# Kernel tuning notes

Hardware: AMD Instinct MI355X
Metric: run time of the kernel (lower is better)

The kernel has to match this reference:

```python
import jax, jax.numpy as jnp
import numpy as np

HEADS = 8
DIM_HEAD = 32
DIM = 256           # must equal HEADS*DIM_HEAD (required by the torch view)
HIDDEN = HEADS * DIM_HEAD
NUM_GROUPS = 32
EPS = 1e-6


def setup_inputs() -> dict:
    key = jax.random.key(0)
    ks = jax.random.split(key, 6)
    b, c, h, w = 16, DIM, 64, 64
    x = jax.random.normal(ks[0], (b, c, h, w), dtype=jnp.float32)
    # conv1x1 weights stored as 2D matrices (out_ch, in_ch)
    w_qkv = jax.random.normal(ks[1], (3 * HIDDEN, DIM), dtype=jnp.float32) * (1.0 / np.sqrt(DIM))
    w_out = jax.random.normal(ks[2], (DIM, HIDDEN), dtype=jnp.float32) * (1.0 / np.sqrt(HIDDEN))
    b_out = jax.random.normal(ks[3], (DIM,), dtype=jnp.float32) * 0.01
    gn_gamma = jnp.ones((DIM,), dtype=jnp.float32)
    gn_beta = jnp.zeros((DIM,), dtype=jnp.float32)
    return {"x": x, "w_qkv": w_qkv, "w_out": w_out, "b_out": b_out,
            "gn_gamma": gn_gamma, "gn_beta": gn_beta}


def _group_norm(x, gamma, beta):
    # GroupNorm32: compute in float32, eps=1e-6, affine
    b, c, h, w = x.shape
    g = NUM_GROUPS
    xf = x.astype(jnp.float32).reshape(b, g, c // g, h, w)
    mean = xf.mean(axis=(2, 3, 4), keepdims=True)
    var = xf.var(axis=(2, 3, 4), keepdims=True)
    xn = (xf - mean) * jax.lax.rsqrt(var + EPS)
    xn = xn.reshape(b, c, h, w)
    return (xn * gamma[None, :, None, None] + beta[None, :, None, None]).astype(x.dtype)


def reference(x, w_qkv, w_out, b_out, gn_gamma, gn_beta):
    b, c, h, w = x.shape
    n = h * w
    # qkv projection (1x1 conv == matmul over channels)
    qkv = jnp.einsum('oc,bchw->bohw', w_qkv, x)            # (b, 3*hidden, h, w)
    qkv = qkv.reshape(b, 3, HEADS, DIM_HEAD, n)
    q, k, v = qkv[:, 0], qkv[:, 1], qkv[:, 2]              # (b, h, d, n)
    q = jax.nn.softmax(q, axis=-2)                         # softmax over feature dim
    k = jax.nn.softmax(k, axis=-1)                         # softmax over spatial dim
    context = jnp.einsum('bhdn,bhen->bhde', k, v)          # (b, heads, d, d)
    out = jnp.einsum('bhde,bhdn->bhen', context, q)        # (b, heads, d, n)
    out = out.reshape(b, c, h, w)
    out = jnp.einsum('oc,bchw->bohw', w_out, out) + b_out[None, :, None, None]
    out = _group_norm(out, gn_gamma, gn_beta)
    return out + x
```

## Files before the change

### kernel.cpp

```cpp
#include <hip/hip_runtime.h>


typedef short s8v __attribute__((ext_vector_type(8)));
typedef float f32x4 __attribute__((ext_vector_type(4)));

__device__ __forceinline__ short f2bf(float f) {
  union { float f; unsigned u; } v; v.f = f;
  unsigned r = v.u + 0x7FFF + ((v.u >> 16) & 1);
  return (short)(r >> 16);
}
__device__ __forceinline__ float bf2f(short h) {
  union { unsigned u; float f; } v; v.u = ((unsigned)(unsigned short)h) << 16;
  return v.f;
}
__device__ __forceinline__ void gld16(const short* g, short* l) {
  __builtin_amdgcn_global_load_lds(
      (const __attribute__((address_space(1))) unsigned*)g,
      (__attribute__((address_space(3))) unsigned*)l, 16, 0, 0);
}

__global__ __launch_bounds__(256) void cast_to_bf16(
    const float* __restrict__ src, short* __restrict__ dst, int n8) {
  int id = blockIdx.x * 256 + threadIdx.x;
  if (id >= n8) return;
  long off = (long)id * 8;
  float4 a = *(const float4*)&src[off];
  float4 b = *(const float4*)&src[off + 4];
  s8v o;
  o[0] = f2bf(a.x); o[1] = f2bf(a.y); o[2] = f2bf(a.z); o[3] = f2bf(a.w);
  o[4] = f2bf(b.x); o[5] = f2bf(b.y); o[6] = f2bf(b.z); o[7] = f2bf(b.w);
  *(s8v*)&dst[off] = o;
}

__global__ __launch_bounds__(256) void cast_transpose_x(
    const float* __restrict__ x, short* __restrict__ xt) {
  int b = blockIdx.z;
  int n0 = blockIdx.x * 64, c0 = blockIdx.y * 64;
  __shared__ short ls[64][65];
  int t = threadIdx.x;
  const float* xb = x + ((long)b * 256 + c0) * 4096 + n0;
  int ci = t >> 4, j4 = (t & 15) * 4;
#pragma unroll
  for (int i = 0; i < 4; ++i) {
    int cl = ci + i * 16;
    float4 v = *(const float4*)&xb[(long)cl * 4096 + j4];
    ls[j4 + 0][cl] = f2bf(v.x);
    ls[j4 + 1][cl] = f2bf(v.y);
    ls[j4 + 2][cl] = f2bf(v.z);
    ls[j4 + 3][cl] = f2bf(v.w);
  }
  __syncthreads();
  short* xtb = xt + ((long)b * 4096 + n0) * 256 + c0;
#pragma unroll
  for (int i = 0; i < 2; ++i) {
    int id = t + i * 256;
    int nl = id >> 3, c8 = (id & 7) * 8;
    s8v o;
#pragma unroll
    for (int e = 0; e < 8; ++e) o[e] = ls[nl][c8 + e];
    *(s8v*)&xtb[(long)nl * 256 + c8] = o;
  }
}

__global__ __launch_bounds__(256) void gemm_bf16(
    const short* __restrict__ A, const short* __restrict__ Bt,
    short* __restrict__ C, const float* __restrict__ bias,
    long a_bstride, int M) {
  __shared__ short lA[128 * 64];
  __shared__ short lB[128 * 64];
  int b = blockIdx.z;
  int mt = blockIdx.y * 128, nt = blockIdx.x * 128;
  int tid = threadIdx.x;
  int lane = tid & 63;
  int wm = tid >> 7, wn = (tid >> 6) & 1;
  const short* Ab = A + (long)b * a_bstride + (long)mt * 256;
  const short* Bb = Bt + ((long)b * 4096 + nt) * 256;
  short* Cb = C + ((long)b * M + mt) * 4096 + nt;

  f32x4 acc[4][4];
#pragma unroll
  for (int i = 0; i < 4; ++i)
#pragma unroll
    for (int j = 0; j < 4; ++j) acc[i][j] = (f32x4){0.f, 0.f, 0.f, 0.f};

  for (int k0 = 0; k0 < 256; k0 += 64) {
#pragma unroll
    for (int is = 0; is < 4; ++is) {
      int s = is * 256 + tid;
      int row = s >> 3, kcp = s & 7;
      int kcl = kcp ^ (row & 7);
      short* la = &lA[(is * 256 + (tid & ~63)) * 8];
      short* lb = &lB[(is * 256 + (tid & ~63)) * 8];
      gld16(Ab + (long)row * 256 + k0 + kcl * 8, la);
      gld16(Bb + (long)row * 256 + k0 + kcl * 8, lb);
    }
    asm volatile("s_waitcnt vmcnt(0)" ::: "memory");
    __syncthreads();
#pragma unroll
    for (int kw = 0; kw < 2; ++kw) {
      int kc = kw * 4 + (lane >> 4);
      int rl = lane & 15;
      s8v av[4], bv[4];
#pragma unroll
      for (int mi = 0; mi < 4; ++mi) {
        int row = wm * 64 + mi * 16 + rl;
        av[mi] = *(const s8v*)&lA[row * 64 + ((kc ^ (row & 7)) << 3)];
      }
#pragma unroll
      for (int ni = 0; ni < 4; ++ni) {
        int row = wn * 64 + ni * 16 + rl;
        bv[ni] = *(const s8v*)&lB[row * 64 + ((kc ^ (row & 7)) << 3)];
      }
#pragma unroll
      for (int mi = 0; mi < 4; ++mi)
#pragma unroll
        for (int ni = 0; ni < 4; ++ni)
          acc[mi][ni] = __builtin_amdgcn_mfma_f32_16x16x32_bf16(
              av[mi], bv[ni], acc[mi][ni], 0, 0, 0);
    }
    __syncthreads();
  }
#pragma unroll
  for (int mi = 0; mi < 4; ++mi) {
#pragma unroll
    for (int r = 0; r < 4; ++r) {
      int o = wm * 64 + mi * 16 + (lane >> 4) * 4 + r;
      float bvv = bias ? bias[mt + o] : 0.f;
#pragma unroll
      for (int ni = 0; ni < 4; ++ni) {
        int n = wn * 64 + ni * 16 + (lane & 15);
        Cb[(long)o * 4096 + n] = f2bf(acc[mi][ni][r] + bvv);
      }
    }
  }
}

__global__ __launch_bounds__(256) void softmax_qT(
    const short* __restrict__ qkv, short* __restrict__ qt) {
  int n = blockIdx.x * 256 + threadIdx.x;
  int h = blockIdx.y, b = blockIdx.z;
  const short* qb = qkv + ((long)b * 768 + h * 32) * 4096 + n;
  float v[32];
  float m = -1e30f;
#pragma unroll
  for (int d = 0; d < 32; ++d) { v[d] = bf2f(qb[(long)d * 4096]); m = fmaxf(m, v[d]); }
  float s = 0.f;
#pragma unroll
  for (int d = 0; d < 32; ++d) { v[d] = __expf(v[d] - m); s += v[d]; }
  float inv = 1.f / s;
  short* dst = qt + ((long)b * 4096 + n) * 256 + h * 32;
#pragma unroll
  for (int c8 = 0; c8 < 4; ++c8) {
    s8v o;
#pragma unroll
    for (int e = 0; e < 8; ++e) o[e] = f2bf(v[c8 * 8 + e] * inv);
    *(s8v*)&dst[c8 * 8] = o;
  }
}

__global__ __launch_bounds__(256) void ctx_mfma(
    const short* __restrict__ qkv, float* __restrict__ ctxp, float* __restrict__ sp) {
  int split = blockIdx.x;
  int h = blockIdx.y, b = blockIdx.z;
  int tid = threadIdx.x;
  int w = tid >> 6, l = tid & 63;
  const short* kb = qkv + ((long)(b * 768 + 256) + h * 32) * 4096;
  const short* vb = kb + (long)256 * 4096;
  int rl = l & 15, kg = l >> 4;
  int n_base = split * 1024 + w * 256;

  f32x4 acc[2][2];
#pragma unroll
  for (int i = 0; i < 2; ++i)
#pragma unroll
    for (int j = 0; j < 2; ++j) acc[i][j] = (f32x4){0.f, 0.f, 0.f, 0.f};
  float s_part0 = 0.f, s_part1 = 0.f;

#pragma unroll 2
  for (int it = 0; it < 8; ++it) {
    int n0 = n_base + it * 32 + kg * 8;
    s8v a0, a1, b0, b1;
    {
      s8v kr = *(const s8v*)&kb[(long)rl * 4096 + n0];
#pragma unroll
      for (int j = 0; j < 8; ++j) {
        float f = __expf(bf2f(kr[j]));
        s_part0 += f;
        a0[j] = f2bf(f);
      }
    }
    {
      s8v kr = *(const s8v*)&kb[(long)(16 + rl) * 4096 + n0];
#pragma unroll
      for (int j = 0; j < 8; ++j) {
        float f = __expf(bf2f(kr[j]));
        s_part1 += f;
        a1[j] = f2bf(f);
      }
    }
    b0 = *(const s8v*)&vb[(long)rl * 4096 + n0];
    b1 = *(const s8v*)&vb[(long)(16 + rl) * 4096 + n0];
    acc[0][0] = __builtin_amdgcn_mfma_f32_16x16x32_bf16(a0, b0, acc[0][0], 0, 0, 0);
    acc[0][1] = __builtin_amdgcn_mfma_f32_16x16x32_bf16(a0, b1, acc[0][1], 0, 0, 0);
    acc[1][0] = __builtin_amdgcn_mfma_f32_16x16x32_bf16(a1, b0, acc[1][0], 0, 0, 0);
    acc[1][1] = __builtin_amdgcn_mfma_f32_16x16x32_bf16(a1, b1, acc[1][1], 0, 0, 0);
  }
  s_part0 += __shfl_xor(s_part0, 16); s_part0 += __shfl_xor(s_part0, 32);
  s_part1 += __shfl_xor(s_part1, 16); s_part1 += __shfl_xor(s_part1, 32);

  __shared__ float lctx[4][1024];
  __shared__ float lsum[4][32];
#pragma unroll
  for (int di = 0; di < 2; ++di)
#pragma unroll
    for (int ei = 0; ei < 2; ++ei)
#pragma unroll
      for (int r = 0; r < 4; ++r) {
        int row = di * 16 + kg * 4 + r;
        int col = ei * 16 + rl;
        lctx[w][row * 32 + col] = acc[di][ei][r];
      }
  if (kg == 0) { lsum[w][rl] = s_part0; lsum[w][16 + rl] = s_part1; }
  __syncthreads();
  long base = (long)(b * 8 + h) * 4 + split;
#pragma unroll
  for (int i = 0; i < 4; ++i) {
    int id = tid + i * 256;
    ctxp[base * 1024 + id] = lctx[0][id] + lctx[1][id] + lctx[2][id] + lctx[3][id];
  }
  if (tid < 32)
    sp[base * 32 + tid] = lsum[0][tid] + lsum[1][tid] + lsum[2][tid] + lsum[3][tid];
}

__global__ __launch_bounds__(256) void make_wf(
    const float* __restrict__ ctxp, const float* __restrict__ sp,
    const float* __restrict__ w_out, short* __restrict__ wf) {
  int h = blockIdx.x, b = blockIdx.y;
  __shared__ float c[32][33];
  __shared__ float inv_s[32];
  __shared__ float wv[256][33];
  int t = threadIdx.x;
  long base = (long)(b * 8 + h) * 4;
#pragma unroll
  for (int i = 0; i < 4; ++i) {
    int id = t + i * 256;
    float v = ctxp[base * 1024 + id] + ctxp[(base + 1) * 1024 + id] +
              ctxp[(base + 2) * 1024 + id] + ctxp[(base + 3) * 1024 + id];
    c[id >> 5][id & 31] = v;
  }
  if (t < 32) {
    float sv = sp[base * 32 + t] + sp[(base + 1) * 32 + t] +
               sp[(base + 2) * 32 + t] + sp[(base + 3) * 32 + t];
    inv_s[t] = 1.f / sv;
  }
#pragma unroll
  for (int r = 0; r < 32; ++r) {
    int row = r * 8 + (t >> 5);
    wv[row][t & 31] = w_out[row * 256 + h * 32 + (t & 31)];
  }
  __syncthreads();
  float wr[32];
#pragma unroll
  for (int e = 0; e < 32; ++e) wr[e] = wv[t][e];
  float tmp[32];
#pragma unroll
  for (int dd = 0; dd < 32; ++dd) {
    float sum = 0.f;
#pragma unroll
    for (int e = 0; e < 32; ++e) sum += wr[e] * c[dd][e];
    tmp[dd] = sum * inv_s[dd];
  }
  short* dst = wf + ((long)b * 256 + t) * 256 + h * 32;
#pragma unroll
  for (int c8 = 0; c8 < 4; ++c8) {
    s8v o;
#pragma unroll
    for (int e = 0; e < 8; ++e) o[e] = f2bf(tmp[c8 * 8 + e]);
    *(s8v*)&dst[c8 * 8] = o;
  }
}

__global__ __launch_bounds__(256) void gn_stats(
    const short* __restrict__ lin, float2* __restrict__ stats) {
  int g = blockIdx.x, b = blockIdx.y;
  const short* base = lin + ((long)b * 256 + g * 8) * 4096;
  int t = threadIdx.x;
  float s = 0.f, ss = 0.f;
#pragma unroll
  for (int l = 0; l < 16; ++l) {
    s8v v = ((const s8v*)base)[t + l * 256];
#pragma unroll
    for (int e = 0; e < 8; ++e) { float f = bf2f(v[e]); s += f; ss += f * f; }
  }
  int wave = t >> 6, lane = t & 63;
#pragma unroll
  for (int off = 32; off >= 1; off >>= 1) { s += __shfl_xor(s, off); ss += __shfl_xor(ss, off); }
  __shared__ float rs[4], rss[4];
  if (lane == 0) { rs[wave] = s; rss[wave] = ss; }
  __syncthreads();
  if (t == 0) {
    s = rs[0] + rs[1] + rs[2] + rs[3];
    ss = rss[0] + rss[1] + rss[2] + rss[3];
    float mean = s * (1.f / 32768.f);
    float var = ss * (1.f / 32768.f) - mean * mean;
    stats[b * 32 + g] = make_float2(mean, rsqrtf(var + 1e-6f));
  }
}

__global__ __launch_bounds__(256) void final_out(
    const short* __restrict__ lin, const float* __restrict__ x,
    const float2* __restrict__ stats, const float* __restrict__ gamma,
    const float* __restrict__ beta, float* __restrict__ out) {
  long id = (long)blockIdx.x * 256 + threadIdx.x;
  long e0 = id * 8;
  int b = (int)(e0 >> 20);
  int rem = (int)(e0 & 1048575);
  int c = rem >> 12;
  float2 st = stats[b * 32 + (c >> 3)];
  float ga = gamma[c] * st.y;
  float be = beta[c] - st.x * ga;
  s8v l8 = *(const s8v*)&lin[e0];
  float4 x0 = *(const float4*)&x[e0];
  float4 x1 = *(const float4*)&x[e0 + 4];
  float4 o0, o1;
  o0.x = bf2f(l8[0]) * ga + be + x0.x;
  o0.y = bf2f(l8[1]) * ga + be + x0.y;
  o0.z = bf2f(l8[2]) * ga + be + x0.z;
  o0.w = bf2f(l8[3]) * ga + be + x0.w;
  o1.x = bf2f(l8[4]) * ga + be + x1.x;
  o1.y = bf2f(l8[5]) * ga + be + x1.y;
  o1.z = bf2f(l8[6]) * ga + be + x1.z;
  o1.w = bf2f(l8[7]) * ga + be + x1.w;
  *(float4*)&out[e0] = o0;
  *(float4*)&out[e0 + 4] = o1;
}

extern "C" void kernel_launch(void* const* d_in, const int* in_sizes, int n_in,
                              void* d_out, int out_size, void* d_ws, size_t ws_size,
                              hipStream_t stream) {
  const float* x     = (const float*)d_in[0];
  const float* w_qkv = (const float*)d_in[1];
  const float* w_out = (const float*)d_in[2];
  const float* b_out = (const float*)d_in[3];
  const float* gamma = (const float*)d_in[4];
  const float* beta  = (const float*)d_in[5];
  float* out = (float*)d_out;

  short* xt   = (short*)d_ws;
  short* qkvb = xt + 16777216;
  short* lin  = qkvb + 50331648;
  short* wqb  = lin + 16777216;
  short* wfb  = wqb + 196608;
  float* ctxp = (float*)(wfb + 1048576);
  float* sp   = ctxp + 524288;
  float2* stats = (float2*)(sp + 16384);

  cast_to_bf16<<<96, 256, 0, stream>>>(w_qkv, wqb, 24576);
  cast_transpose_x<<<dim3(64, 4, 16), 256, 0, stream>>>(x, xt);
  gemm_bf16<<<dim3(32, 6, 16), 256, 0, stream>>>(wqb, xt, qkvb, nullptr, 0, 768);
  softmax_qT<<<dim3(16, 8, 16), 256, 0, stream>>>(qkvb, xt);
  ctx_mfma<<<dim3(4, 8, 16), 256, 0, stream>>>(qkvb, ctxp, sp);
  make_wf<<<dim3(8, 16), 256, 0, stream>>>(ctxp, sp, w_out, wfb);
  gemm_bf16<<<dim3(32, 2, 16), 256, 0, stream>>>(wfb, xt, lin, b_out, 65536, 256);
  gn_stats<<<dim3(32, 16), 256, 0, stream>>>(lin, stats);
  final_out<<<8192, 256, 0, stream>>>(lin, x, stats, gamma, beta, out);
}
```

Measured before the change: 157.9 us.

## Fuse q-softmax into QKV GEMM epilogue and GroupNorm stats into output GEMM

The QKV GEMM now applies the feature-dim softmax to q tiles in its epilogue, using lane shuffles, and writes transposed q directly. This removes the separate softmax_qT pass and the write and re-read of q. The output GEMM accumulates GroupNorm sum and sum-of-squares with atomics in its epilogue, which replaces the gn_stats kernel; final_out now derives mean and rstd from those sums. Both GEMMs also double-buffer their LDS staging so global loads overlap the MFMA work. The costs are more LDS per block, nondeterministic atomic accumulation order, and an extra zeroing kernel.

Result: slower. 161.9 us (+2.5%).

```diff
diff --git a/kernel.cpp b/kernel.cpp
--- a/kernel.cpp
+++ b/kernel.cpp
@@ -32,6 +32,10 @@
   *(s8v*)&dst[off] = o;
 }
 
+__global__ __launch_bounds__(256) void zero_stats(float* __restrict__ p) {
+  p[blockIdx.x * 256 + threadIdx.x] = 0.f;
+}
+
 __global__ __launch_bounds__(256) void cast_transpose_x(
     const float* __restrict__ x, short* __restrict__ xt) {
   int b = blockIdx.z;
@@ -62,20 +66,19 @@
   }
 }
 
-__global__ __launch_bounds__(256) void gemm_bf16(
+__global__ __launch_bounds__(256) void gemm_qkv(
     const short* __restrict__ A, const short* __restrict__ Bt,
-    short* __restrict__ C, const float* __restrict__ bias,
-    long a_bstride, int M) {
-  __shared__ short lA[128 * 64];
-  __shared__ short lB[128 * 64];
+    short* __restrict__ kv, short* __restrict__ qT) {
+  __shared__ short lA[2][8192];
+  __shared__ short lB[2][8192];
   int b = blockIdx.z;
   int mt = blockIdx.y * 128, nt = blockIdx.x * 128;
   int tid = threadIdx.x;
   int lane = tid & 63;
   int wm = tid >> 7, wn = (tid >> 6) & 1;
-  const short* Ab = A + (long)b * a_bstride + (long)mt * 256;
+  int rl = lane & 15, kg = lane >> 4;
+  const short* Ab = A + (long)mt * 256;
   const short* Bb = Bt + ((long)b * 4096 + nt) * 256;
-  short* Cb = C + ((long)b * M + mt) * 4096 + nt;
 
   f32x4 acc[4][4];
 #pragma unroll
@@ -83,33 +86,41 @@
 #pragma unroll
     for (int j = 0; j < 4; ++j) acc[i][j] = (f32x4){0.f, 0.f, 0.f, 0.f};
 
-  for (int k0 = 0; k0 < 256; k0 += 64) {
+  auto stage = [&](int buf, int k0) {
 #pragma unroll
     for (int is = 0; is < 4; ++is) {
       int s = is * 256 + tid;
       int row = s >> 3, kcp = s & 7;
       int kcl = kcp ^ (row & 7);
-      short* la = &lA[(is * 256 + (tid & ~63)) * 8];
-      short* lb = &lB[(is * 256 + (tid & ~63)) * 8];
-      gld16(Ab + (long)row * 256 + k0 + kcl * 8, la);
-      gld16(Bb + (long)row * 256 + k0 + kcl * 8, lb);
-    }
-    asm volatile("s_waitcnt vmcnt(0)" ::: "memory");
-    __syncthreads();
+      gld16(Ab + (long)row * 256 + k0 + kcl * 8, &lA[buf][(is * 256 + (tid & ~63)) * 8]);
+      gld16(Bb + (long)row * 256 + k0 + kcl * 8, &lB[buf][(is * 256 + (tid & ~63)) * 8]);
+    }
+  };
+
+  stage(0, 0);
+#pragma unroll
+  for (int s = 0; s < 4; ++s) {
+    int cur = s & 1;
+    if (s < 3) {
+      stage(cur ^ 1, (s + 1) * 64);
+      asm volatile("s_waitcnt vmcnt(8)" ::: "memory");
+    } else {
+      asm volatile("s_waitcnt vmcnt(0)" ::: "memory");
+    }
+    __builtin_amdgcn_s_barrier();
 #pragma unroll
     for (int kw = 0; kw < 2; ++kw) {
-      int kc = kw * 4 + (lane >> 4);
-      int rl = lane & 15;
+      int kc = kw * 4 + kg;
       s8v av[4], bv[4];
 #pragma unroll
       for (int mi = 0; mi < 4; ++mi) {
         int row = wm * 64 + mi * 16 + rl;
-        av[mi] = *(const s8v*)&lA[row * 64 + ((kc ^ (row & 7)) << 3)];
+        av[mi] = *(const s8v*)&lA[cur][row * 64 + ((kc ^ (row & 7)) << 3)];
       }
 #pragma unroll
       for (int ni = 0; ni < 4; ++ni) {
         int row = wn * 64 + ni * 16 + rl;
-        bv[ni] = *(const s8v*)&lB[row * 64 + ((kc ^ (row & 7)) << 3)];
+        bv[ni] = *(const s8v*)&lB[cur][row * 64 + ((kc ^ (row & 7)) << 3)];
       }
 #pragma unroll
       for (int mi = 0; mi < 4; ++mi)
@@ -118,53 +129,170 @@
           acc[mi][ni] = __builtin_amdgcn_mfma_f32_16x16x32_bf16(
               av[mi], bv[ni], acc[mi][ni], 0, 0, 0);
     }
-    __syncthreads();
-  }
+    asm volatile("s_waitcnt lgkmcnt(0)" ::: "memory");
+    __builtin_amdgcn_s_barrier();
+  }
+
+  if (mt < 256) {
+    short* qTb = qT + ((long)b * 4096 + nt) * 256 + mt;
+#pragma unroll
+    for (int ni = 0; ni < 4; ++ni) {
+      int n = wn * 64 + ni * 16 + rl;
+#pragma unroll
+      for (int p = 0; p < 2; ++p) {
+        float v[8];
+        float m = -1e30f;
+#pragma unroll
+        for (int j = 0; j < 8; ++j) {
+          v[j] = acc[p * 2 + (j >> 2)][ni][j & 3];
+          m = fmaxf(m, v[j]);
+        }
+        m = fmaxf(m, __shfl_xor(m, 16));
+        m = fmaxf(m, __shfl_xor(m, 32));
+        float ssum = 0.f;
+#pragma unroll
+        for (int j = 0; j < 8; ++j) { v[j] = __expf(v[j] - m); ssum += v[j]; }
+        ssum += __shfl_xor(ssum, 16);
+        ssum += __shfl_xor(ssum, 32);
+        float inv = 1.f / ssum;
+#pragma unroll
+        for (int half = 0; half < 2; ++half) {
+          short4 o;
+          o.x = f2bf(v[half * 4 + 0] * inv);
+          o.y = f2bf(v[half * 4 + 1] * inv);
+          o.z = f2bf(v[half * 4 + 2] * inv);
+          o.w = f2bf(v[half * 4 + 3] * inv);
+          *(short4*)&qTb[(long)n * 256 + wm * 64 + p * 32 + half * 16 + kg * 4] = o;
+        }
+      }
+    }
+  } else {
+    short* Cb = kv + ((long)b * 512 + (mt - 256)) * 4096 + nt;
+#pragma unroll
+    for (int mi = 0; mi < 4; ++mi) {
+#pragma unroll
+      for (int r = 0; r < 4; ++r) {
+        int o = wm * 64 + mi * 16 + kg * 4 + r;
+#pragma unroll
+        for (int ni = 0; ni < 4; ++ni) {
+          int n = wn * 64 + ni * 16 + rl;
+          Cb[(long)o * 4096 + n] = f2bf(acc[mi][ni][r]);
+        }
+      }
+    }
+  }
+}
+
+__global__ __launch_bounds__(256) void gemm_lin(
+    const short* __restrict__ A, const short* __restrict__ Bt,
+    short* __restrict__ C, const float* __restrict__ bias,
+    float* __restrict__ st2) {
+  __shared__ short lA[2][8192];
+  __shared__ short lB[2][8192];
+  int b = blockIdx.z;
+  int mt = blockIdx.y * 128, nt = blockIdx.x * 128;
+  int tid = threadIdx.x;
+  int lane = tid & 63;
+  int wm = tid >> 7, wn = (tid >> 6) & 1;
+  int rl = lane & 15, kg = lane >> 4;
+  const short* Ab = A + (long)b * 65536 + (long)mt * 256;
+  const short* Bb = Bt + ((long)b * 4096 + nt) * 256;
+
+  f32x4 acc[4][4];
+#pragma unroll
+  for (int i = 0; i < 4; ++i)
+#pragma unroll
+    for (int j = 0; j < 4; ++j) acc[i][j] = (f32x4){0.f, 0.f, 0.f, 0.f};
+
+  auto stage = [&](int buf, int k0) {
+#pragma unroll
+    for (int is = 0; is < 4; ++is) {
+      int s = is * 256 + tid;
+      int row = s >> 3, kcp = s & 7;
+      int kcl = kcp ^ (row & 7);
+      gld16(Ab + (long)row * 256 + k0 + kcl * 8, &lA[buf][(is * 256 + (tid & ~63)) * 8]);
+      gld16(Bb + (long)row * 256 + k0 + kcl * 8, &lB[buf][(is * 256 + (tid & ~63)) * 8]);
+    }
+  };
+
+  stage(0, 0);
+#pragma unroll
+  for (int s = 0; s < 4; ++s) {
+    int cur = s & 1;
+    if (s < 3) {
+      stage(cur ^ 1, (s + 1) * 64);
+      asm volatile("s_waitcnt vmcnt(8)" ::: "memory");
+    } else {
+      asm volatile("s_waitcnt vmcnt(0)" ::: "memory");
+    }
+    __builtin_amdgcn_s_barrier();
+#pragma unroll
+    for (int kw = 0; kw < 2; ++kw) {
+      int kc = kw * 4 + kg;
+      s8v av[4], bv[4];
+#pragma unroll
+      for (int mi = 0; mi < 4; ++mi) {
+        int row = wm * 64 + mi * 16 + rl;
+        av[mi] = *(const s8v*)&lA[cur][row * 64 + ((kc ^ (row & 7)) << 3)];
+      }
+#pragma unroll
+      for (int ni = 0; ni < 4; ++ni) {
+        int row = wn * 64 + ni * 16 + rl;
+        bv[ni] = *(const s8v*)&lB[cur][row * 64 + ((kc ^ (row & 7)) << 3)];
+      }
+#pragma unroll
+      for (int mi = 0; mi < 4; ++mi)
+#pragma unroll
+        for (int ni = 0; ni < 4; ++ni)
+          acc[mi][ni] = __builtin_amdgcn_mfma_f32_16x16x32_bf16(
+              av[mi], bv[ni], acc[mi][ni], 0, 0, 0);
+    }
+    asm volatile("s_waitcnt lgkmcnt(0)" ::: "memory");
+    __builtin_amdgcn_s_barrier();
+  }
+
+  short* Cb = C + ((long)b * 256 + mt) * 4096 + nt;
+  float s1[4] = {0.f, 0.f, 0.f, 0.f};
+  float s2[4] = {0.f, 0.f, 0.f, 0.f};
 #pragma unroll
   for (int mi = 0; mi < 4; ++mi) {
 #pragma unroll
     for (int r = 0; r < 4; ++r) {
-      int o = wm * 64 + mi * 16 + (lane >> 4) * 4 + r;
-      float bvv = bias ? bias[mt + o] : 0.f;
+      int o = wm * 64 + mi * 16 + kg * 4 + r;
+      float bv = bias[mt + o];
 #pragma unroll
       for (int ni = 0; ni < 4; ++ni) {
-        int n = wn * 64 + ni * 16 + (lane & 15);
-        Cb[(long)o * 4096 + n] = f2bf(acc[mi][ni][r] + bvv);
-      }
-    }
-  }
-}
-
-__global__ __launch_bounds__(256) void softmax_qT(
-    const short* __restrict__ qkv, short* __restrict__ qt) {
-  int n = blockIdx.x * 256 + threadIdx.x;
-  int h = blockIdx.y, b = blockIdx.z;
-  const short* qb = qkv + ((long)b * 768 + h * 32) * 4096 + n;
-  float v[32];
-  float m = -1e30f;
-#pragma unroll
-  for (int d = 0; d < 32; ++d) { v[d] = bf2f(qb[(long)d * 4096]); m = fmaxf(m, v[d]); }
-  float s = 0.f;
-#pragma unroll
-  for (int d = 0; d < 32; ++d) { v[d] = __expf(v[d] - m); s += v[d]; }
-  float inv = 1.f / s;
-  short* dst = qt + ((long)b * 4096 + n) * 256 + h * 32;
-#pragma unroll
-  for (int c8 = 0; c8 < 4; ++c8) {
-    s8v o;
-#pragma unroll
-    for (int e = 0; e < 8; ++e) o[e] = f2bf(v[c8 * 8 + e] * inv);
-    *(s8v*)&dst[c8 * 8] = o;
+        int n = wn * 64 + ni * 16 + rl;
+        short h = f2bf(acc[mi][ni][r] + bv);
+        Cb[(long)o * 4096 + n] = h;
+        float q = bf2f(h);
+        s1[mi] += q;
+        s2[mi] += q * q;
+      }
+    }
+  }
+#pragma unroll
+  for (int mi = 0; mi < 4; ++mi) {
+#pragma unroll
+    for (int off = 1; off <= 16; off <<= 1) {
+      s1[mi] += __shfl_xor(s1[mi], off);
+      s2[mi] += __shfl_xor(s2[mi], off);
+    }
+    if (rl == 0 && (kg & 1) == 0) {
+      int g = (mt >> 3) + wm * 8 + mi * 2 + (kg >> 1);
+      atomicAdd(&st2[(b * 32 + g) * 2], s1[mi]);
+      atomicAdd(&st2[(b * 32 + g) * 2 + 1], s2[mi]);
+    }
   }
 }
 
 __global__ __launch_bounds__(256) void ctx_mfma(
-    const short* __restrict__ qkv, float* __restrict__ ctxp, float* __restrict__ sp) {
+    const short* __restrict__ kv, float* __restrict__ ctxp, float* __restrict__ sp) {
   int split = blockIdx.x;
   int h = blockIdx.y, b = blockIdx.z;
   int tid = threadIdx.x;
   int w = tid >> 6, l = tid & 63;
-  const short* kb = qkv + ((long)(b * 768 + 256) + h * 32) * 4096;
+  const short* kb = kv + ((long)(b * 512) + h * 32) * 4096;
   const short* vb = kb + (long)256 * 4096;
   int rl = l & 15, kg = l >> 4;
   int n_base = split * 1024 + w * 256;
@@ -280,45 +408,20 @@
   }
 }
 
-__global__ __launch_bounds__(256) void gn_stats(
-    const short* __restrict__ lin, float2* __restrict__ stats) {
-  int g = blockIdx.x, b = blockIdx.y;
-  const short* base = lin + ((long)b * 256 + g * 8) * 4096;
-  int t = threadIdx.x;
-  float s = 0.f, ss = 0.f;
-#pragma unroll
-  for (int l = 0; l < 16; ++l) {
-    s8v v = ((const s8v*)base)[t + l * 256];
-#pragma unroll
-    for (int e = 0; e < 8; ++e) { float f = bf2f(v[e]); s += f; ss += f * f; }
-  }
-  int wave = t >> 6, lane = t & 63;
-#pragma unroll
-  for (int off = 32; off >= 1; off >>= 1) { s += __shfl_xor(s, off); ss += __shfl_xor(ss, off); }
-  __shared__ float rs[4], rss[4];
-  if (lane == 0) { rs[wave] = s; rss[wave] = ss; }
-  __syncthreads();
-  if (t == 0) {
-    s = rs[0] + rs[1] + rs[2] + rs[3];
-    ss = rss[0] + rss[1] + rss[2] + rss[3];
-    float mean = s * (1.f / 32768.f);
-    float var = ss * (1.f / 32768.f) - mean * mean;
-    stats[b * 32 + g] = make_float2(mean, rsqrtf(var + 1e-6f));
-  }
-}
-
 __global__ __launch_bounds__(256) void final_out(
     const short* __restrict__ lin, const float* __restrict__ x,
-    const float2* __restrict__ stats, const float* __restrict__ gamma,
+    const float2* __restrict__ st2, const float* __restrict__ gamma,
     const float* __restrict__ beta, float* __restrict__ out) {
   long id = (long)blockIdx.x * 256 + threadIdx.x;
   long e0 = id * 8;
   int b = (int)(e0 >> 20);
   int rem = (int)(e0 & 1048575);
   int c = rem >> 12;
-  float2 st = stats[b * 32 + (c >> 3)];
-  float ga = gamma[c] * st.y;
-  float be = beta[c] - st.x * ga;
+  float2 st = st2[b * 32 + (c >> 3)];
+  float mean = st.x * (1.f / 32768.f);
+  float inv = rsqrtf(st.y * (1.f / 32768.f) - mean * mean + 1e-6f);
+  float ga = gamma[c] * inv;
+  float be = beta[c] - mean * ga;
   s8v l8 = *(const s8v*)&lin[e0];
   float4 x0 = *(const float4*)&x[e0];
   float4 x1 = *(const float4*)&x[e0 + 4];
@@ -347,21 +450,21 @@
   float* out = (float*)d_out;
 
   short* xt   = (short*)d_ws;
-  short* qkvb = xt + 16777216;
-  short* lin  = qkvb + 50331648;
+  short* qT   = xt + 16777216;
+  short* kvb  = qT + 16777216;
+  short* lin  = kvb + 33554432;
   short* wqb  = lin + 16777216;
   short* wfb  = wqb + 196608;
   float* ctxp = (float*)(wfb + 1048576);
   float* sp   = ctxp + 524288;
-  float2* stats = (float2*)(sp + 16384);
+  float* st2  = sp + 16384;
 
   cast_to_bf16<<<96, 256, 0, stream>>>(w_qkv, wqb, 24576);
+  zero_stats<<<4, 256, 0, stream>>>(st2);
   cast_transpose_x<<<dim3(64, 4, 16), 256, 0, stream>>>(x, xt);
-  gemm_bf16<<<dim3(32, 6, 16), 256, 0, stream>>>(wqb, xt, qkvb, nullptr, 0, 768);
-  softmax_qT<<<dim3(16, 8, 16), 256, 0, stream>>>(qkvb, xt);
-  ctx_mfma<<<dim3(4, 8, 16), 256, 0, stream>>>(qkvb, ctxp, sp);
+  gemm_qkv<<<dim3(32, 6, 16), 256, 0, stream>>>(wqb, xt, kvb, qT);
+  ctx_mfma<<<dim3(4, 8, 16), 256, 0, stream>>>(kvb, ctxp, sp);
   make_wf<<<dim3(8, 16), 256, 0, stream>>>(ctxp, sp, w_out, wfb);
-  gemm_bf16<<<dim3(32, 2, 16), 256, 0, stream>>>(wfb, xt, lin, b_out, 65536, 256);
-  gn_stats<<<dim3(32, 16), 256, 0, stream>>>(lin, stats);
-  final_out<<<8192, 256, 0, stream>>>(lin, x, stats, gamma, beta, out);
-}
+  gemm_lin<<<dim3(32, 2, 16), 256, 0, stream>>>(wfb, qT, lin, b_out, st2);
+  final_out<<<8192, 256, 0, stream>>>(lin, x, (const float2*)st2, gamma, beta, out);
+}
```
